# Kernel tuning notes

Measured on AMD Instinct MI355X. Metric: run time of the kernel, lower is better.

Reference implementation:

```python
import jax, jax.numpy as jnp
import numpy as np

DIM = 1024        # BIGNET_DIM
GROUP = 16        # Linear4Bit group_size
LORA = 20         # lora_dim hardcoded in Block
NLAYERS = 18      # 6 blocks * 3 QLoRALinear
NBLOCKS = 6
BATCH = 8192
EPS = 1e-5


def setup_inputs() -> dict:
    key = jax.random.key(0)
    ks = jax.random.split(key, 6)
    x = jax.random.normal(ks[0], (BATCH, DIM), jnp.float32)
    # int4 quantized base weights in [-8, 7], stored as int32
    qw = jax.random.randint(ks[1], (NLAYERS, DIM, DIM), -8, 8, jnp.int32)
    # per-(out_row, input-group) dequant scales
    scales = jax.random.uniform(ks[2], (NLAYERS, DIM, DIM // GROUP), jnp.float32,
                                minval=0.005, maxval=0.02)
    bias = jax.random.normal(ks[3], (NLAYERS, DIM), jnp.float32) * 0.01
    # lora_a: kaiming-uniform-like scale; lora_b: small nonzero (zeros in torch init,
    # randomized here so the LoRA path is numerically exercised)
    lora_a = jax.random.normal(ks[4], (NLAYERS, LORA, DIM), jnp.float32) / np.sqrt(DIM)
    lora_b = jax.random.normal(ks[5], (NLAYERS, DIM, LORA), jnp.float32) * 0.01
    ln_w = jnp.ones((NBLOCKS - 1, DIM), jnp.float32)
    ln_b = jnp.zeros((NBLOCKS - 1, DIM), jnp.float32)
    return dict(x=x, qw=qw, scales=scales, bias=bias,
                lora_a=lora_a, lora_b=lora_b, ln_w=ln_w, ln_b=ln_b)


def _qlora_linear(x, qw, sc, b, A, B):
    # dequantize: each group of 16 input cols of a row shares one scale
    w = (qw.astype(jnp.float32).reshape(DIM, DIM // GROUP, GROUP)
         * sc[:, :, None]).reshape(DIM, DIM)          # [out, in]
    base = x @ w.T + b                                # [N, out]
    lora = (x @ A.T) @ B.T                            # [N, r] @ [r, out]
    return base + lora


def _layernorm(x, w, b):
    m = jnp.mean(x, axis=-1, keepdims=True)
    v = jnp.mean((x - m) ** 2, axis=-1, keepdims=True)
    return (x - m) * jax.lax.rsqrt(v + EPS) * w + b


def reference(x, qw, scales, bias, lora_a, lora_b, ln_w, ln_b):
    h = x
    li = 0
    for blk in range(NBLOCKS):
        r = h
        for j in range(3):
            r = _qlora_linear(r, qw[li], scales[li], bias[li], lora_a[li], lora_b[li])
            if j < 2:
                r = jax.nn.relu(r)
            li += 1
        h = h + r  # residual
        if blk < NBLOCKS - 1:
            h = _layernorm(h, ln_w[blk], ln_b[blk])
    return h
```

## Files before the change

kernel.cpp:

```cpp
#include <hip/hip_runtime.h>
#include <cstdint>
#include <cstddef>

#define DIM      1024
#define GROUP    16
#define LORA     20
#define NLAYERS  18
#define NBLOCKS  6
#define BATCH    8192
#define EPS      1e-5f

typedef __bf16 bf16_8 __attribute__((ext_vector_type(8)));
typedef __bf16 bf16_4 __attribute__((ext_vector_type(4)));
typedef float  f32x4  __attribute__((ext_vector_type(4)));

__global__ __launch_bounds__(256, 3) void wprep_kernel(
    const int* __restrict__ qw, const float* __restrict__ sc,
    const float* __restrict__ la, const float* __restrict__ lb,
    __bf16* __restrict__ whi) {
  const int l  = blockIdx.x >> 7;
  const int og = (blockIdx.x >> 1) & 63;
  const int cg = blockIdx.x & 1;
  const int tid = threadIdx.x;
  const int tc = tid & 31;
  const int tr = tid >> 5;

  int4  q[2][4];
  float sv[2][4];
  size_t rowb[2];
#pragma unroll
  for (int u = 0; u < 2; ++u) {
    const int orow = og * 16 + tr * 2 + u;
    rowb[u] = ((size_t)l * DIM + orow) * DIM + cg * 512;
    const size_t scb = ((size_t)l * DIM + orow) * (DIM / GROUP) + cg * 32;
#pragma unroll
    for (int v = 0; v < 4; ++v) {
      const int c = v * 128 + tc * 4;
      q[u][v] = *(const int4*)&qw[rowb[u] + c];
      sv[u][v] = sc[scb + (c >> 4)];
    }
  }

  __shared__ float As[10 * 512];
  __shared__ float Bs[16 * LORA];

  const float* Abase = la + (size_t)l * LORA * DIM + cg * 512;
  const float* Bbase = lb + ((size_t)l * DIM + og * 16) * LORA;
  for (int i = tid; i < 16 * LORA; i += 256) Bs[i] = Bbase[i];
#pragma unroll
  for (int i = 0; i < 5; ++i) {
    const int f4 = i * 256 + tid;
    ((float4*)As)[f4] = *(const float4*)(Abase + (size_t)(f4 >> 7) * DIM + (f4 & 127) * 4);
  }
  __syncthreads();

  float acc[2][16];
#pragma unroll
  for (int u = 0; u < 2; ++u)
#pragma unroll
    for (int v = 0; v < 4; ++v) {
      acc[u][v * 4 + 0] = q[u][v].x * sv[u][v];
      acc[u][v * 4 + 1] = q[u][v].y * sv[u][v];
      acc[u][v * 4 + 2] = q[u][v].z * sv[u][v];
      acc[u][v * 4 + 3] = q[u][v].w * sv[u][v];
    }

#pragma unroll 1
  for (int half = 0; half < 2; ++half) {
    if (half == 1) {
      __syncthreads();
#pragma unroll
      for (int i = 0; i < 5; ++i) {
        const int f4 = i * 256 + tid;
        ((float4*)As)[f4] =
            *(const float4*)(Abase + (size_t)(10 + (f4 >> 7)) * DIM + (f4 & 127) * 4);
      }
      __syncthreads();
    }
#pragma unroll 2
    for (int jj = 0; jj < 10; ++jj) {
      const int j = half * 10 + jj;
      float4 a[4];
#pragma unroll
      for (int v = 0; v < 4; ++v)
        a[v] = *(const float4*)&As[jj * 512 + v * 128 + tc * 4];
#pragma unroll
      for (int u = 0; u < 2; ++u) {
        const float bj = Bs[(tr * 2 + u) * LORA + j];
#pragma unroll
        for (int v = 0; v < 4; ++v) {
          acc[u][v * 4 + 0] += bj * a[v].x;
          acc[u][v * 4 + 1] += bj * a[v].y;
          acc[u][v * 4 + 2] += bj * a[v].z;
          acc[u][v * 4 + 3] += bj * a[v].w;
        }
      }
    }
  }

#pragma unroll
  for (int u = 0; u < 2; ++u) {
#pragma unroll
    for (int v = 0; v < 4; ++v) {
      const bf16_4 hv = {(__bf16)acc[u][v * 4 + 0], (__bf16)acc[u][v * 4 + 1],
                         (__bf16)acc[u][v * 4 + 2], (__bf16)acc[u][v * 4 + 3]};
      *(bf16_4*)&whi[rowb[u] + v * 128 + tc * 4] = hv;
    }
  }
}

__global__ __launch_bounds__(256) void xprep_kernel(
    const float* __restrict__ x, __bf16* __restrict__ hi) {
  const size_t i = (size_t)blockIdx.x * 256 + threadIdx.x;
  const float4 v = ((const float4*)x)[i];
  const bf16_4 hv = {(__bf16)v.x, (__bf16)v.y, (__bf16)v.z, (__bf16)v.w};
  ((bf16_4*)hi)[i] = hv;
}

#define GBUF    12288
#define GOFF_W  8192

template <int NISSUE>
__device__ __forceinline__ void stageR(const __bf16* __restrict__ g, int row0, int k0,
                                       __bf16* lds, int tid) {
#pragma unroll
  for (int i = 0; i < NISSUE; ++i) {
    const int D = i * 8192 + tid * 16;
    const int r  = D >> 6;
    const int ce = (D & 63) >> 1;
    const __bf16* gp = g + (size_t)(row0 + r) * DIM + k0 + ce;
    __builtin_amdgcn_global_load_lds(
        (const __attribute__((address_space(1))) void*)gp,
        (__attribute__((address_space(3))) void*)(lds + i * 4096 + (tid >> 6) * 512), 16, 0, 0);
  }
}

template <int MODE>
__global__ __launch_bounds__(512, 1) void gemm1_kernel(
    const __bf16* __restrict__ X, const __bf16* __restrict__ Wh,
    const float* __restrict__ bias, __bf16* __restrict__ Oh,
    const float* __restrict__ Hin,
    const float2* __restrict__ stats,
    const float* __restrict__ lnw, const float* __restrict__ lnb,
    float* __restrict__ Sout) {
  __shared__ __bf16 smem[4 * GBUF];

  const int tid  = threadIdx.x;
  const int lane = tid & 63;
  const int wv   = tid >> 6;
  const int wm   = wv >> 2;
  const int wn2  = wv & 3;
  const int xcd = blockIdx.x & 7;
  const int kk  = blockIdx.x >> 3;
  const int tm  = xcd * 4 + (kk >> 3);
  const int tn  = kk & 7;
  const int rowX = tm * 256, rowW = tn * 128;

  const int lr   = lane & 15;
  const int slot = lane >> 4;

  int offX[4], offW[4];
#pragma unroll
  for (int n = 0; n < 4; ++n) offX[n] = (wn2 * 64 + n * 16 + lr) * 32 + slot * 8;
#pragma unroll
  for (int m = 0; m < 4; ++m) offW[m] = GOFF_W + (wm * 64 + m * 16 + lr) * 32 + slot * 8;

  f32x4 acc[4][4];
#pragma unroll
  for (int m = 0; m < 4; ++m)
#pragma unroll
    for (int n = 0; n < 4; ++n) acc[m][n] = f32x4{0.f, 0.f, 0.f, 0.f};

  auto stage_tile = [&](int t) {
    __bf16* sb = smem + (t & 3) * GBUF;
    stageR<2>(X,  rowX, t * 32, sb, tid);
    stageR<1>(Wh, rowW, t * 32, sb + GOFF_W, tid);
  };

  auto compute_tile = [&](int t) {
    const __bf16* buf = smem + (t & 3) * GBUF;
    bf16_8 xf[4];
#pragma unroll
    for (int n = 0; n < 4; ++n) xf[n] = *(const bf16_8*)&buf[offX[n]];
#pragma unroll
    for (int m = 0; m < 4; ++m) {
      const bf16_8 w_h = *(const bf16_8*)&buf[offW[m]];
#pragma unroll
      for (int n = 0; n < 4; ++n)
        acc[m][n] = __builtin_amdgcn_mfma_f32_16x16x32_bf16(w_h, xf[n], acc[m][n], 0, 0, 0);
    }
  };

  stage_tile(0); stage_tile(1); stage_tile(2);
  asm volatile("s_waitcnt vmcnt(6)" ::: "memory");
  __builtin_amdgcn_s_barrier();

#pragma unroll 1
  for (int kt = 0; kt < 29; ++kt) {
    stage_tile(kt + 3);
    compute_tile(kt);
    asm volatile("s_waitcnt vmcnt(6)" ::: "memory");
    __builtin_amdgcn_s_barrier();
  }
  compute_tile(29);
  asm volatile("s_waitcnt vmcnt(3)" ::: "memory");
  __builtin_amdgcn_s_barrier();
  compute_tile(30);
  asm volatile("s_waitcnt vmcnt(0)" ::: "memory");
  __builtin_amdgcn_s_barrier();
  compute_tile(31);

  const int g4 = slot * 4;
#pragma unroll
  for (int m = 0; m < 4; ++m) {
    const int feat = tn * 128 + wm * 64 + m * 16 + g4;
    const float4 bv = *(const float4*)&bias[feat];
    float4 wq, bq;
    if constexpr (MODE == 2) {
      wq = *(const float4*)&lnw[feat];
      bq = *(const float4*)&lnb[feat];
    }
#pragma unroll
    for (int n = 0; n < 4; ++n) {
      const int nb = tm * 256 + wn2 * 64 + n * 16 + lr;
      const size_t base = (size_t)nb * DIM + feat;
      float v0 = acc[m][n][0] + bv.x;
      float v1 = acc[m][n][1] + bv.y;
      float v2 = acc[m][n][2] + bv.z;
      float v3 = acc[m][n][3] + bv.w;
      if constexpr (MODE == 0) {
        const bf16_4 hv = {(__bf16)fmaxf(v0, 0.f), (__bf16)fmaxf(v1, 0.f),
                           (__bf16)fmaxf(v2, 0.f), (__bf16)fmaxf(v3, 0.f)};
        *(bf16_4*)&Oh[base] = hv;
      } else if constexpr (MODE == 1) {
        const float4 h = *(const float4*)&Hin[base];
        *(float4*)&Sout[base] = float4{v0 + h.x, v1 + h.y, v2 + h.z, v3 + h.w};
      } else {
        const float2 st = stats[nb];
        const float4 s = *(const float4*)&Hin[base];
        const float h0 = (s.x - st.x) * st.y * wq.x + bq.x;
        const float h1 = (s.y - st.x) * st.y * wq.y + bq.y;
        const float h2 = (s.z - st.x) * st.y * wq.z + bq.z;
        const float h3 = (s.w - st.x) * st.y * wq.w + bq.w;
        *(float4*)&Sout[base] = float4{v0 + h0, v1 + h1, v2 + h2, v3 + h3};
      }
    }
  }
}

__global__ __launch_bounds__(256) void normcast_kernel(
    const float* __restrict__ S, const float* __restrict__ w,
    const float* __restrict__ b, float2* __restrict__ stats,
    __bf16* __restrict__ phi) {
  const int row = blockIdx.x;
  const int tid = threadIdx.x;
  const int lane = tid & 63;
  const int wv = tid >> 6;
  const float4 v = ((const float4*)(S + (size_t)row * DIM))[tid];

  float s = v.x + v.y + v.z + v.w;
#pragma unroll
  for (int m = 32; m; m >>= 1) s += __shfl_xor(s, m, 64);
  __shared__ float red[8];
  if (lane == 0) red[wv] = s;
  __syncthreads();
  const float mean = (red[0] + red[1] + red[2] + red[3]) * (1.f / DIM);

  const float d0 = v.x - mean, d1 = v.y - mean, d2 = v.z - mean, d3 = v.w - mean;
  float q = d0 * d0 + d1 * d1 + d2 * d2 + d3 * d3;
#pragma unroll
  for (int m = 32; m; m >>= 1) q += __shfl_xor(q, m, 64);
  if (lane == 0) red[4 + wv] = q;
  __syncthreads();
  const float var = (red[4] + red[5] + red[6] + red[7]) * (1.f / DIM);
  const float inv = 1.f / sqrtf(var + EPS);

  if (tid == 0) stats[row] = float2{mean, inv};

  const float4 wv4 = ((const float4*)w)[tid];
  const float4 bv4 = ((const float4*)b)[tid];
  const bf16_4 hv = {(__bf16)(d0 * inv * wv4.x + bv4.x),
                     (__bf16)(d1 * inv * wv4.y + bv4.y),
                     (__bf16)(d2 * inv * wv4.z + bv4.z),
                     (__bf16)(d3 * inv * wv4.w + bv4.w)};
  ((bf16_4*)phi)[(size_t)row * (DIM / 4) + tid] = hv;
}

extern "C" void kernel_launch(void* const* d_in, const int* in_sizes, int n_in,
                              void* d_out, int out_size, void* d_ws, size_t ws_size,
                              hipStream_t stream) {
  const float* x   = (const float*)d_in[0];
  const int*   qw  = (const int*)d_in[1];
  const float* sc  = (const float*)d_in[2];
  const float* bias= (const float*)d_in[3];
  const float* la  = (const float*)d_in[4];
  const float* lb  = (const float*)d_in[5];
  const float* lnw = (const float*)d_in[6];
  const float* lnb = (const float*)d_in[7];
  float* out = (float*)d_out;
  char* ws = (char*)d_ws;

  __bf16* WHI = (__bf16*)(ws);
  __bf16* X0  = (__bf16*)(ws + 37748736);
  __bf16* X1  = (__bf16*)(ws + 54525952);
  float*  SA  = (float*)(ws + 71303168);
  float*  SB  = (float*)(ws + 104857600);
  float2* STT = (float2*)(ws + 138412032);
  (void)ws_size; (void)in_sizes; (void)n_in; (void)out_size;

  xprep_kernel<<<BATCH * DIM / (256 * 4), 256, 0, stream>>>(x, X0);
  wprep_kernel<<<NLAYERS * 128, 256, 0, stream>>>(qw, sc, la, lb, WHI);

  const dim3 ggrid(BATCH / 256 * (DIM / 128));
  for (int blk = 0; blk < NBLOCKS; ++blk) {
    const int li = blk * 3;
    const size_t w0 = (size_t)li * DIM * DIM;
    const size_t w1 = (size_t)(li + 1) * DIM * DIM;
    const size_t w2 = (size_t)(li + 2) * DIM * DIM;
    float* Scur = (blk & 1) ? SB : SA;
    float* Sprev = (blk & 1) ? SA : SB;

    gemm1_kernel<0><<<ggrid, 512, 0, stream>>>(
        X0, WHI + w0, bias + (size_t)li * DIM, X1,
        nullptr, nullptr, nullptr, nullptr, nullptr);
    gemm1_kernel<0><<<ggrid, 512, 0, stream>>>(
        X1, WHI + w1, bias + (size_t)(li + 1) * DIM, X0,
        nullptr, nullptr, nullptr, nullptr, nullptr);
    float* sout = (blk == NBLOCKS - 1) ? out : Scur;
    if (blk == 0) {
      gemm1_kernel<1><<<ggrid, 512, 0, stream>>>(
          X0, WHI + w2, bias + (size_t)(li + 2) * DIM, nullptr,
          x, nullptr, nullptr, nullptr, sout);
    } else {
      gemm1_kernel<2><<<ggrid, 512, 0, stream>>>(
          X0, WHI + w2, bias + (size_t)(li + 2) * DIM, nullptr,
          Sprev, STT, lnw + (size_t)(blk - 1) * DIM, lnb + (size_t)(blk - 1) * DIM,
          sout);
    }
    if (blk < NBLOCKS - 1) {
      normcast_kernel<<<BATCH, 256, 0, stream>>>(
          Scur, lnw + (size_t)blk * DIM, lnb + (size_t)blk * DIM, STT, X0);
    }
  }
}
```

Measured before the change: 553.7 us.

## Double K-tile depth to 64 with XOR-swizzled LDS layout, 3-stage ring

The GEMM's K-tile grows from 32 to 64, so each stage loads twice as much and the main loop runs half as many iterations and barriers. The ring buffer drops from four stages to three. An XOR swizzle on the 128-byte LDS rows is applied at the global-load address and at the fragment reads, to avoid LDS bank conflicts in the wider layout. This trades shallower prefetch depth and a larger LDS footprint for fewer synchronisations per K.

```diff
diff --git a/kernel.cpp b/kernel.cpp
--- a/kernel.cpp
+++ b/kernel.cpp
@@ -117,8 +117,13 @@
   ((bf16_4*)hi)[i] = hv;
 }
 
-#define GBUF    12288
-#define GOFF_W  8192
+#define GBUF    24576
+#define GOFF_W  16384
+
+__device__ __forceinline__ int swz_off(int row, int slot) {
+  const int colb = (slot * 16) ^ ((row & 7) << 4);
+  return (row * 128 + colb) >> 1;
+}
 
 template <int NISSUE>
 __device__ __forceinline__ void stageR(const __bf16* __restrict__ g, int row0, int k0,
@@ -126,9 +131,9 @@
 #pragma unroll
   for (int i = 0; i < NISSUE; ++i) {
     const int D = i * 8192 + tid * 16;
-    const int r  = D >> 6;
-    const int ce = (D & 63) >> 1;
-    const __bf16* gp = g + (size_t)(row0 + r) * DIM + k0 + ce;
+    const int row = D >> 7;
+    const int colb = (D & 127) ^ ((row & 7) << 4);
+    const __bf16* gp = g + (size_t)(row0 + row) * DIM + k0 + (colb >> 1);
     __builtin_amdgcn_global_load_lds(
         (const __attribute__((address_space(1))) void*)gp,
         (__attribute__((address_space(3))) void*)(lds + i * 4096 + (tid >> 6) * 512), 16, 0, 0);
@@ -143,7 +148,7 @@
     const float2* __restrict__ stats,
     const float* __restrict__ lnw, const float* __restrict__ lnb,
     float* __restrict__ Sout) {
-  __shared__ __bf16 smem[4 * GBUF];
+  __shared__ __bf16 smem[3 * GBUF];
 
   const int tid  = threadIdx.x;
   const int lane = tid & 63;
@@ -151,9 +156,9 @@
   const int wm   = wv >> 2;
   const int wn2  = wv & 3;
   const int xcd = blockIdx.x & 7;
-  const int kk  = blockIdx.x >> 3;
-  const int tm  = xcd * 4 + (kk >> 3);
-  const int tn  = kk & 7;
+  const int kk2 = blockIdx.x >> 3;
+  const int tm  = xcd * 4 + (kk2 >> 3);
+  const int tn  = kk2 & 7;
   const int rowX = tm * 256, rowW = tn * 128;
 
   const int lr   = lane & 15;
@@ -161,9 +166,9 @@
 
   int offX[4], offW[4];
 #pragma unroll
-  for (int n = 0; n < 4; ++n) offX[n] = (wn2 * 64 + n * 16 + lr) * 32 + slot * 8;
-#pragma unroll
-  for (int m = 0; m < 4; ++m) offW[m] = GOFF_W + (wm * 64 + m * 16 + lr) * 32 + slot * 8;
+  for (int n = 0; n < 4; ++n) offX[n] = swz_off(wn2 * 64 + n * 16 + lr, slot);
+#pragma unroll
+  for (int m = 0; m < 4; ++m) offW[m] = GOFF_W + swz_off(wm * 64 + m * 16 + lr, slot);
 
   f32x4 acc[4][4];
 #pragma unroll
@@ -172,43 +177,44 @@
     for (int n = 0; n < 4; ++n) acc[m][n] = f32x4{0.f, 0.f, 0.f, 0.f};
 
   auto stage_tile = [&](int t) {
-    __bf16* sb = smem + (t & 3) * GBUF;
-    stageR<2>(X,  rowX, t * 32, sb, tid);
-    stageR<1>(Wh, rowW, t * 32, sb + GOFF_W, tid);
+    __bf16* sb = smem + (t % 3) * GBUF;
+    stageR<4>(X,  rowX, t * 64, sb, tid);
+    stageR<2>(Wh, rowW, t * 64, sb + GOFF_W, tid);
   };
 
   auto compute_tile = [&](int t) {
-    const __bf16* buf = smem + (t & 3) * GBUF;
-    bf16_8 xf[4];
-#pragma unroll
-    for (int n = 0; n < 4; ++n) xf[n] = *(const bf16_8*)&buf[offX[n]];
-#pragma unroll
-    for (int m = 0; m < 4; ++m) {
-      const bf16_8 w_h = *(const bf16_8*)&buf[offW[m]];
-#pragma unroll
-      for (int n = 0; n < 4; ++n)
-        acc[m][n] = __builtin_amdgcn_mfma_f32_16x16x32_bf16(w_h, xf[n], acc[m][n], 0, 0, 0);
+    const __bf16* buf = smem + (t % 3) * GBUF;
+#pragma unroll
+    for (int kk = 0; kk < 2; ++kk) {
+      const int kx = kk * 32;
+      bf16_8 xf[4];
+#pragma unroll
+      for (int n = 0; n < 4; ++n) xf[n] = *(const bf16_8*)&buf[offX[n] ^ kx];
+#pragma unroll
+      for (int m = 0; m < 4; ++m) {
+        const bf16_8 w_h = *(const bf16_8*)&buf[offW[m] ^ kx];
+#pragma unroll
+        for (int n = 0; n < 4; ++n)
+          acc[m][n] = __builtin_amdgcn_mfma_f32_16x16x32_bf16(w_h, xf[n], acc[m][n], 0, 0, 0);
+      }
     }
   };
 
-  stage_tile(0); stage_tile(1); stage_tile(2);
+  stage_tile(0); stage_tile(1);
   asm volatile("s_waitcnt vmcnt(6)" ::: "memory");
   __builtin_amdgcn_s_barrier();
 
 #pragma unroll 1
-  for (int kt = 0; kt < 29; ++kt) {
-    stage_tile(kt + 3);
+  for (int kt = 0; kt < 14; ++kt) {
+    stage_tile(kt + 2);
     compute_tile(kt);
     asm volatile("s_waitcnt vmcnt(6)" ::: "memory");
     __builtin_amdgcn_s_barrier();
   }
-  compute_tile(29);
-  asm volatile("s_waitcnt vmcnt(3)" ::: "memory");
-  __builtin_amdgcn_s_barrier();
-  compute_tile(30);
+  compute_tile(14);
   asm volatile("s_waitcnt vmcnt(0)" ::: "memory");
   __builtin_amdgcn_s_barrier();
-  compute_tile(31);
+  compute_tile(15);
 
   const int g4 = slot * 4;
 #pragma unroll
```

New measurement: 527.8 us. 1.05x faster.
